# Kernel optimization log

Measured on AMD Instinct MI355X. Metric: run time of the kernel, lower is better.

## Reference

```python
import jax, jax.numpy as jnp
import numpy as np

B, T, C, H = 2, 2048, 1024, 16
D = C // H  # 64 per-head dim


def setup_inputs() -> dict:
    key = jax.random.key(0)
    ks = jax.random.split(key, 9)
    s = 1.0 / np.sqrt(C)
    return {
        "query_src": jax.random.normal(ks[0], (B, T, C), jnp.float32),
        "key_src": jax.random.normal(ks[1], (B, T, C), jnp.float32),
        "value_src": jax.random.normal(ks[2], (B, T, C), jnp.float32),
        "Wq": jax.random.normal(ks[3], (C, C), jnp.float32) * s,
        "Wk": jax.random.normal(ks[4], (C, C), jnp.float32) * s,
        "Wv": jax.random.normal(ks[5], (C, C), jnp.float32) * s,
        "Wo": jax.random.normal(ks[6], (C, C), jnp.float32) * s,
        "bo": jax.random.normal(ks[7], (C,), jnp.float32) * s,
    }


def reference(query_src, key_src, value_src, Wq, Wk, Wv, Wo, bo):
    # Linear layers: y = x @ W.T (torch nn.Linear convention)
    q = jnp.einsum('btc,dc->btd', query_src, Wq).reshape(B, T, H, D).transpose(0, 2, 1, 3)
    k = jnp.einsum('btc,dc->btd', key_src, Wk).reshape(B, T, H, D).transpose(0, 2, 1, 3)
    v = jnp.einsum('btc,dc->btd', value_src, Wv).reshape(B, T, H, D).transpose(0, 2, 1, 3)
    # scores: [B, H, T, T]
    scores = jnp.einsum('bhqd,bhkd->bhqk', q, k)
    # FAITHFUL quirk: original divides by d**(-0.5) => multiplies by sqrt(D)
    scores = scores * jnp.sqrt(jnp.asarray(D, scores.dtype))
    # FAITHFUL quirk: softmax over dim=1 == the HEAD axis
    attn = jax.nn.softmax(scores, axis=1)
    # dropout is identity in eval mode
    out = jnp.einsum('bhqk,bhkd->bhqd', attn, v)  # [B,H,T,D]
    out = out.transpose(0, 2, 1, 3).reshape(B, T, C)
    return jnp.einsum('btc,dc->btd', out, Wo) + bo
```

## Files before the change

### kernel.cpp

```cpp
#include <hip/hip_runtime.h>
#include <cmath>

namespace {

constexpr int B_ = 2;
constexpr int T_ = 2048;
constexpr int C_ = 1024;
constexpr int H_ = 16;
constexpr int D_ = 64;

typedef _Float16 half8 __attribute__((ext_vector_type(8)));
typedef _Float16 half4 __attribute__((ext_vector_type(4)));
typedef float f32x4 __attribute__((ext_vector_type(4)));

__device__ inline f32x4 vmax4(f32x4 a, f32x4 b) {
  f32x4 r;
  r[0] = fmaxf(a[0], b[0]); r[1] = fmaxf(a[1], b[1]);
  r[2] = fmaxf(a[2], b[2]); r[3] = fmaxf(a[3], b[3]);
  return r;
}

__device__ __forceinline__ void gload16(const _Float16* g, _Float16* l) {
  __builtin_amdgcn_global_load_lds(
      (const __attribute__((address_space(1))) unsigned int*)g,
      (__attribute__((address_space(3))) unsigned int*)l, 16, 0, 0);
}

__global__ __launch_bounds__(256)
void cast7(const float* __restrict__ xq, const float* __restrict__ xk,
           const float* __restrict__ xv, const float* __restrict__ wq,
           const float* __restrict__ wk, const float* __restrict__ wv,
           const float* __restrict__ wo,
           _Float16* __restrict__ dxq, _Float16* __restrict__ dxk,
           _Float16* __restrict__ dxv, _Float16* __restrict__ dwq,
           _Float16* __restrict__ dwk, _Float16* __restrict__ dwv,
           _Float16* __restrict__ dwo) {
  constexpr size_t NX = (size_t)4 << 20;
  constexpr size_t NW = (size_t)1 << 20;
  size_t g = ((size_t)blockIdx.x * 256 + threadIdx.x) * 8;
  const float* s; _Float16* d; size_t off;
  if      (g <     NX)          { s = xq; d = dxq; off = g; }
  else if (g < 2 * NX)          { s = xk; d = dxk; off = g - NX; }
  else if (g < 3 * NX)          { s = xv; d = dxv; off = g - 2 * NX; }
  else if (g < 3 * NX + NW)     { s = wq; d = dwq; off = g - 3 * NX; }
  else if (g < 3 * NX + 2 * NW) { s = wk; d = dwk; off = g - 3 * NX - NW; }
  else if (g < 3 * NX + 3 * NW) { s = wv; d = dwv; off = g - 3 * NX - 2 * NW; }
  else                          { s = wo; d = dwo; off = g - 3 * NX - 3 * NW; }
  const float4 a = *(const float4*)(s + off);
  const float4 b = *(const float4*)(s + off + 4);
  half8 h;
  h[0] = (_Float16)a.x; h[1] = (_Float16)a.y; h[2] = (_Float16)a.z; h[3] = (_Float16)a.w;
  h[4] = (_Float16)b.x; h[5] = (_Float16)b.y; h[6] = (_Float16)b.z; h[7] = (_Float16)b.w;
  *(half8*)(d + off) = h;
}

__global__ __launch_bounds__(256, 3)
void gemm_f16nt(const _Float16* __restrict__ A0, const _Float16* __restrict__ A1,
                const _Float16* __restrict__ A2,
                const _Float16* __restrict__ W0, const _Float16* __restrict__ W1,
                const _Float16* __restrict__ W2,
                _Float16* __restrict__ Y0, _Float16* __restrict__ Y1,
                _Float16* __restrict__ Y2,
                float* __restrict__ Yf, const float* __restrict__ bias,
                int K, int N, int mode) {
  __shared__ _Float16 sA[128 * 32];
  __shared__ _Float16 sW[128 * 32];

  const int tid  = threadIdx.x;
  const int lane = tid & 63;
  const int w    = tid >> 6;
  const int l15  = lane & 15;
  const int quad = lane >> 4;
  const int z    = blockIdx.z;
  const _Float16* A = (z == 0) ? A0 : (z == 1) ? A1 : A2;
  const _Float16* W = (z == 0) ? W0 : (z == 1) ? W1 : W2;
  _Float16*       Y = (z == 0) ? Y0 : (z == 1) ? Y1 : Y2;

  const int m0 = blockIdx.y * 128;
  const int n0 = blockIdx.x * 128;

  const int Rb  = lane >> 2;
  const int pch = lane & 3;
  const int lch = pch ^ ((Rb >> 1) & 3);
  const int swr = (l15 >> 1) & 3;

  f32x4 acc[4][4];
#pragma unroll
  for (int mt = 0; mt < 4; ++mt)
#pragma unroll
    for (int nt = 0; nt < 4; ++nt)
      acc[mt][nt] = (f32x4){0.f, 0.f, 0.f, 0.f};

  const int wm = (w >> 1) * 64;
  const int wn = (w & 1) * 64;

  for (int k0 = 0; k0 < K; k0 += 32) {
    __syncthreads();
#pragma unroll
    for (int j = 0; j < 2; ++j) {
      const int seg = w * 32 + j * 16;
      gload16(A + (size_t)(m0 + seg + Rb) * K + k0 + lch * 8, &sA[seg * 32]);
      gload16(W + (size_t)(n0 + seg + Rb) * K + k0 + lch * 8, &sW[seg * 32]);
    }
    __syncthreads();

    half8 af[4], wf[4];
#pragma unroll
    for (int mt = 0; mt < 4; ++mt) {
      const int R = wm + mt * 16 + l15;
      af[mt] = *(const half8*)&sA[R * 32 + (quad ^ swr) * 8];
    }
#pragma unroll
    for (int nt = 0; nt < 4; ++nt) {
      const int R = wn + nt * 16 + l15;
      wf[nt] = *(const half8*)&sW[R * 32 + (quad ^ swr) * 8];
    }
#pragma unroll
    for (int mt = 0; mt < 4; ++mt)
#pragma unroll
      for (int nt = 0; nt < 4; ++nt)
        acc[mt][nt] = __builtin_amdgcn_mfma_f32_16x16x32_f16(wf[nt], af[mt], acc[mt][nt], 0, 0, 0);
  }

#pragma unroll
  for (int mt = 0; mt < 4; ++mt)
#pragma unroll
    for (int nt = 0; nt < 4; ++nt) {
      const int m = m0 + wm + mt * 16 + l15;
      const int n = n0 + wn + nt * 16 + quad * 4;
      if (mode == 2) {
        float4 v;
        v.x = acc[mt][nt][0] + bias[n + 0];
        v.y = acc[mt][nt][1] + bias[n + 1];
        v.z = acc[mt][nt][2] + bias[n + 2];
        v.w = acc[mt][nt][3] + bias[n + 3];
        *(float4*)(Yf + (size_t)m * N + n) = v;
      } else {
        half4 hv;
#pragma unroll
        for (int r = 0; r < 4; ++r) hv[r] = (_Float16)acc[mt][nt][r];
        *(half4*)(Y + (size_t)m * N + n) = hv;
      }
    }
}

__global__ __launch_bounds__(256)
void transpose_v(const _Float16* __restrict__ Vh, _Float16* __restrict__ Vt) {
  constexpr int PAD = 1028;
  __shared__ _Float16 tile[16][PAD];
  const int b  = blockIdx.x >> 7;
  const int kt = blockIdx.x & 127;
  const int tid = threadIdx.x;

#pragma unroll
  for (int j = 0; j < 8; ++j) {
    const int ch = tid + 256 * j;
    const int t  = ch >> 7;
    const int c8 = ch & 127;
    *(half8*)&tile[t][c8 * 8] =
        *(const half8*)(Vh + ((size_t)b * T_ + kt * 16 + t) * C_ + c8 * 8);
  }
  __syncthreads();

#pragma unroll
  for (int j = 0; j < 8; ++j) {
    const int cc = tid + 256 * j;
    const int h  = cc >> 7;
    const int d  = (cc >> 1) & 63;
    const int th = (cc & 1) * 8;
    half8 v;
#pragma unroll
    for (int i = 0; i < 8; ++i) v[i] = tile[th + i][h * 64 + d];
    *(half8*)(Vt + ((((size_t)b * H_ + h) * 128 + kt) * 64 + d) * 16 + th) = v;
  }
}

__global__ __launch_bounds__(256, 2)
void attn_mfma(const _Float16* __restrict__ Qhp, const _Float16* __restrict__ Khp,
               const _Float16* __restrict__ Vtp, _Float16* __restrict__ OP,
               int nsplit) {
  __shared__ f32x4 red[2][2][4][64];

  const int tid  = threadIdx.x;
  const int lane = tid & 63;
  const int w    = tid >> 6;
  const int l15  = lane & 15;
  const int quad = lane >> 4;
  const int cell = quad * 16 + l15;

  const int nbq   = B_ * (T_ / 16);
  const int split = blockIdx.x / nbq;
  const int bq    = blockIdx.x % nbq;
  const int b  = bq >> 7;
  const int q0 = (bq & 127) << 4;

  const size_t qrow = ((size_t)b * T_ + q0 + l15) * C_;

  half8 qh[4][2];
#pragma unroll
  for (int hl = 0; hl < 4; ++hl)
#pragma unroll
    for (int kk = 0; kk < 2; ++kk)
      qh[hl][kk] = *(const half8*)(Qhp + qrow + (w * 4 + hl) * 64 + kk * 32 + quad * 8);

  f32x4 oacc[4][4];
#pragma unroll
  for (int hl = 0; hl < 4; ++hl)
#pragma unroll
    for (int mt = 0; mt < 4; ++mt)
      oacc[hl][mt] = (f32x4){0.f, 0.f, 0.f, 0.f};

  const int kpb  = T_ / nsplit;
  const int k_lo = split * kpb;
  const int jt   = kpb / 16;

  for (int j = 0; j < jt; ++j) {
    const int k0 = k_lo + j * 16;
    const int p  = j & 1;
    const int kt = k0 >> 4;
    const size_t krow = ((size_t)b * T_ + k0 + l15) * C_;

    half8 akh[4][2];
    half4 avf[4][4];
#pragma unroll
    for (int hl = 0; hl < 4; ++hl)
#pragma unroll
      for (int kk = 0; kk < 2; ++kk)
        akh[hl][kk] = *(const half8*)(Khp + krow + (w * 4 + hl) * 64 + kk * 32 + quad * 8);
#pragma unroll
    for (int hl = 0; hl < 4; ++hl) {
      const _Float16* vb =
          Vtp + (((size_t)b * H_ + (w * 4 + hl)) * 128 + kt) * 1024;
#pragma unroll
      for (int mt = 0; mt < 4; ++mt)
        avf[hl][mt] = *(const half4*)(vb + (mt * 16 + l15) * 16 + quad * 4);
    }

    f32x4 s[4];
#pragma unroll
    for (int hl = 0; hl < 4; ++hl) s[hl] = (f32x4){0.f, 0.f, 0.f, 0.f};
#pragma unroll
    for (int hl = 0; hl < 4; ++hl)
#pragma unroll
      for (int kk = 0; kk < 2; ++kk)
        s[hl] = __builtin_amdgcn_mfma_f32_16x16x32_f16(akh[hl][kk], qh[hl][kk], s[hl], 0, 0, 0);
#pragma unroll
    for (int hl = 0; hl < 4; ++hl) s[hl] = s[hl] * 8.f;

    red[p][0][w][cell] = vmax4(vmax4(s[0], s[1]), vmax4(s[2], s[3]));
    __syncthreads();
    const f32x4 gmax = vmax4(vmax4(red[p][0][0][cell], red[p][0][1][cell]),
                             vmax4(red[p][0][2][cell], red[p][0][3][cell]));
    float e[4][4];
    f32x4 ps = (f32x4){0.f, 0.f, 0.f, 0.f};
#pragma unroll
    for (int hl = 0; hl < 4; ++hl)
#pragma unroll
      for (int r = 0; r < 4; ++r) {
        e[hl][r] = __expf(s[hl][r] - gmax[r]);
        ps[r] += e[hl][r];
      }
    red[p][1][w][cell] = ps;
    __syncthreads();
    const f32x4 gs = red[p][1][0][cell] + red[p][1][1][cell] +
                     red[p][1][2][cell] + red[p][1][3][cell];
    f32x4 inv;
#pragma unroll
    for (int r = 0; r < 4; ++r) inv[r] = 1.f / gs[r];

    half4 pf[4];
#pragma unroll
    for (int hl = 0; hl < 4; ++hl)
#pragma unroll
      for (int r = 0; r < 4; ++r)
        pf[hl][r] = (_Float16)(e[hl][r] * inv[r]);

#pragma unroll
    for (int hl = 0; hl < 4; ++hl)
#pragma unroll
      for (int mt = 0; mt < 4; ++mt)
        oacc[hl][mt] =
            __builtin_amdgcn_mfma_f32_16x16x16f16(avf[hl][mt], pf[hl], oacc[hl][mt], 0, 0, 0);
  }

  _Float16* op = OP + (size_t)split * ((size_t)B_ * T_ * C_);
  const size_t orow = ((size_t)b * T_ + q0 + l15) * C_;
#pragma unroll
  for (int hl = 0; hl < 4; ++hl)
#pragma unroll
    for (int mt = 0; mt < 4; ++mt) {
      half4 hv;
#pragma unroll
      for (int r = 0; r < 4; ++r) hv[r] = (_Float16)oacc[hl][mt][r];
      *(half4*)(op + orow + (w * 4 + hl) * 64 + mt * 16 + quad * 4) = hv;
    }
}

__global__ __launch_bounds__(256)
void reduce_oh(const _Float16* __restrict__ OP, _Float16* __restrict__ AOh,
               int nsplit, size_t n) {
  const size_t i = ((size_t)blockIdx.x * 256 + threadIdx.x) * 8;
  float a[8] = {};
  for (int s = 0; s < nsplit; ++s) {
    const half8 v = *(const half8*)(OP + (size_t)s * n + i);
#pragma unroll
    for (int r = 0; r < 8; ++r) a[r] += (float)v[r];
  }
  half8 o;
#pragma unroll
  for (int r = 0; r < 8; ++r) o[r] = (_Float16)a[r];
  *(half8*)(AOh + i) = o;
}

}

extern "C" void kernel_launch(void* const* d_in, const int* in_sizes, int n_in,
                              void* d_out, int out_size, void* d_ws, size_t ws_size,
                              hipStream_t stream) {
  const float* xq = (const float*)d_in[0];
  const float* xk = (const float*)d_in[1];
  const float* xv = (const float*)d_in[2];
  const float* Wq = (const float*)d_in[3];
  const float* Wk = (const float*)d_in[4];
  const float* Wv = (const float*)d_in[5];
  const float* Wo = (const float*)d_in[6];
  const float* bo = (const float*)d_in[7];
  float* out = (float*)d_out;

  const size_t MB   = 1ull << 20;
  const size_t nBTC = (size_t)B_ * T_ * C_;

  char* wsb = (char*)d_ws;
  _Float16* Qh  = (_Float16*)(wsb + 0 * MB);
  _Float16* Kh  = (_Float16*)(wsb + 8 * MB);
  _Float16* Vt  = (_Float16*)(wsb + 16 * MB);
  _Float16* vh  = (_Float16*)(wsb + 24 * MB);
  _Float16* AOh = (_Float16*)(wsb + 24 * MB);
  _Float16* xqh = (_Float16*)(wsb + 32 * MB);
  _Float16* xkh = (_Float16*)(wsb + 40 * MB);
  _Float16* xvh = (_Float16*)(wsb + 48 * MB);
  _Float16* OP  = (_Float16*)(wsb + 32 * MB);
  _Float16* Wqh = (_Float16*)(wsb + 64 * MB);
  _Float16* Wkh = (_Float16*)(wsb + 66 * MB);
  _Float16* Wvh = (_Float16*)(wsb + 68 * MB);
  _Float16* Woh = (_Float16*)(wsb + 70 * MB);

  const int nsplit = 4;
  const int M = B_ * T_;
  dim3 blk(256);

  cast7<<<dim3(8192), blk, 0, stream>>>(xq, xk, xv, Wq, Wk, Wv, Wo,
                                        xqh, xkh, xvh, Wqh, Wkh, Wvh, Woh);

  gemm_f16nt<<<dim3(C_ / 128, M / 128, 3), blk, 0, stream>>>(
      xqh, xkh, xvh, Wqh, Wkh, Wvh, Qh, Kh, vh,
      nullptr, nullptr, C_, C_, 0);

  transpose_v<<<dim3(B_ * 128), blk, 0, stream>>>(vh, Vt);

  attn_mfma<<<dim3(B_ * (T_ / 16) * nsplit), blk, 0, stream>>>(Qh, Kh, Vt, OP, nsplit);

  reduce_oh<<<dim3((unsigned)(nBTC / 2048)), blk, 0, stream>>>(OP, AOh, nsplit, nBTC);

  gemm_f16nt<<<dim3(C_ / 128, M / 128, 1), blk, 0, stream>>>(
      AOh, nullptr, nullptr, Woh, nullptr, nullptr, nullptr, nullptr, nullptr,
      out, bo, C_, C_, 2);
}
```

Measured before the change: 390.8 us.

## Prefetch K tiles, repack V^T for 16-byte loads, and prioritize MFMA

Restructures the attention main loop to double-buffer K-tile register loads, issuing the next tile's loads before the softmax reductions so their latency overlaps the barriers. The V transpose kernel now writes a permuted layout so each lane fetches its four 16x16 V fragments with two 16-byte loads instead of sixteen 8-byte loads. It also adds s_setprio around the MFMA blocks and reuses the score registers for the exponentials. The extra buffer raises register pressure, and the unrolled-by-two loop assumes an even tile count per split.

```diff
diff --git a/kernel.cpp b/kernel.cpp
--- a/kernel.cpp
+++ b/kernel.cpp
@@ -168,10 +168,16 @@
     const int h  = cc >> 7;
     const int d  = (cc >> 1) & 63;
     const int th = (cc & 1) * 8;
-    half8 v;
-#pragma unroll
-    for (int i = 0; i < 8; ++i) v[i] = tile[th + i][h * 64 + d];
-    *(half8*)(Vt + ((((size_t)b * H_ + h) * 128 + kt) * 64 + d) * 16 + th) = v;
+    const int c  = h * 64 + d;
+    half4 va, vb4;
+#pragma unroll
+    for (int i = 0; i < 4; ++i) va[i]  = tile[th + i][c];
+#pragma unroll
+    for (int i = 0; i < 4; ++i) vb4[i] = tile[th + 4 + i][c];
+    const size_t base = (((size_t)b * H_ + h) * 128 + kt) * 1024 +
+                        (size_t)((d & 15) * 64 + (th >> 2) * 16 + (d >> 4) * 4);
+    *(half4*)(Vt + base) = va;
+    *(half4*)(Vt + base + 16) = vb4;
   }
 }
 
@@ -214,51 +220,61 @@
   const int k_lo = split * kpb;
   const int jt   = kpb / 16;
 
-  for (int j = 0; j < jt; ++j) {
+  const _Float16* vbase = Vtp + ((size_t)b * H_ + w * 4) * (128 * 1024) +
+                          (size_t)(l15 * 64 + quad * 16);
+
+  half8 akA[4][2], akB[4][2];
+
+  auto loadK = [&](half8 (&buf)[4][2], int k0) {
+    const size_t krow = ((size_t)b * T_ + k0 + l15) * C_;
+#pragma unroll
+    for (int hl = 0; hl < 4; ++hl)
+#pragma unroll
+      for (int kk = 0; kk < 2; ++kk)
+        buf[hl][kk] = *(const half8*)(Khp + krow + (w * 4 + hl) * 64 + kk * 32 + quad * 8);
+  };
+
+  auto tile = [&](int j, half8 (&cur)[4][2], half8 (&nxt)[4][2]) {
     const int k0 = k_lo + j * 16;
+    const int kt = k0 >> 4;
     const int p  = j & 1;
-    const int kt = k0 >> 4;
-    const size_t krow = ((size_t)b * T_ + k0 + l15) * C_;
-
-    half8 akh[4][2];
-    half4 avf[4][4];
+
+    f32x4 s[4];
+#pragma unroll
+    for (int hl = 0; hl < 4; ++hl) s[hl] = (f32x4){0.f, 0.f, 0.f, 0.f};
+    __builtin_amdgcn_s_setprio(1);
 #pragma unroll
     for (int hl = 0; hl < 4; ++hl)
 #pragma unroll
       for (int kk = 0; kk < 2; ++kk)
-        akh[hl][kk] = *(const half8*)(Khp + krow + (w * 4 + hl) * 64 + kk * 32 + quad * 8);
+        s[hl] = __builtin_amdgcn_mfma_f32_16x16x32_f16(cur[hl][kk], qh[hl][kk], s[hl], 0, 0, 0);
+    __builtin_amdgcn_s_setprio(0);
+#pragma unroll
+    for (int hl = 0; hl < 4; ++hl) s[hl] = s[hl] * 8.f;
+
+    half8 avh[4][2];
 #pragma unroll
     for (int hl = 0; hl < 4; ++hl) {
-      const _Float16* vb =
-          Vtp + (((size_t)b * H_ + (w * 4 + hl)) * 128 + kt) * 1024;
-#pragma unroll
-      for (int mt = 0; mt < 4; ++mt)
-        avf[hl][mt] = *(const half4*)(vb + (mt * 16 + l15) * 16 + quad * 4);
-    }
-
-    f32x4 s[4];
-#pragma unroll
-    for (int hl = 0; hl < 4; ++hl) s[hl] = (f32x4){0.f, 0.f, 0.f, 0.f};
-#pragma unroll
-    for (int hl = 0; hl < 4; ++hl)
-#pragma unroll
-      for (int kk = 0; kk < 2; ++kk)
-        s[hl] = __builtin_amdgcn_mfma_f32_16x16x32_f16(akh[hl][kk], qh[hl][kk], s[hl], 0, 0, 0);
-#pragma unroll
-    for (int hl = 0; hl < 4; ++hl) s[hl] = s[hl] * 8.f;
+      const _Float16* vb = vbase + (size_t)hl * (128 * 1024) + (size_t)kt * 1024;
+      avh[hl][0] = *(const half8*)(vb);
+      avh[hl][1] = *(const half8*)(vb + 8);
+    }
+    __builtin_amdgcn_sched_barrier(0);
+    if (j + 1 < jt) loadK(nxt, k0 + 16);
+    __builtin_amdgcn_sched_barrier(0);
 
     red[p][0][w][cell] = vmax4(vmax4(s[0], s[1]), vmax4(s[2], s[3]));
     __syncthreads();
     const f32x4 gmax = vmax4(vmax4(red[p][0][0][cell], red[p][0][1][cell]),
                              vmax4(red[p][0][2][cell], red[p][0][3][cell]));
-    float e[4][4];
     f32x4 ps = (f32x4){0.f, 0.f, 0.f, 0.f};
 #pragma unroll
     for (int hl = 0; hl < 4; ++hl)
 #pragma unroll
       for (int r = 0; r < 4; ++r) {
-        e[hl][r] = __expf(s[hl][r] - gmax[r]);
-        ps[r] += e[hl][r];
+        const float ev = __expf(s[hl][r] - gmax[r]);
+        s[hl][r] = ev;
+        ps[r] += ev;
       }
     red[p][1][w][cell] = ps;
     __syncthreads();
@@ -273,14 +289,27 @@
     for (int hl = 0; hl < 4; ++hl)
 #pragma unroll
       for (int r = 0; r < 4; ++r)
-        pf[hl][r] = (_Float16)(e[hl][r] * inv[r]);
-
-#pragma unroll
-    for (int hl = 0; hl < 4; ++hl)
-#pragma unroll
-      for (int mt = 0; mt < 4; ++mt)
-        oacc[hl][mt] =
-            __builtin_amdgcn_mfma_f32_16x16x16f16(avf[hl][mt], pf[hl], oacc[hl][mt], 0, 0, 0);
+        pf[hl][r] = (_Float16)(s[hl][r] * inv[r]);
+
+    __builtin_amdgcn_s_setprio(1);
+#pragma unroll
+    for (int hl = 0; hl < 4; ++hl) {
+      const half4 v0 = __builtin_shufflevector(avh[hl][0], avh[hl][0], 0, 1, 2, 3);
+      const half4 v1 = __builtin_shufflevector(avh[hl][0], avh[hl][0], 4, 5, 6, 7);
+      const half4 v2 = __builtin_shufflevector(avh[hl][1], avh[hl][1], 0, 1, 2, 3);
+      const half4 v3 = __builtin_shufflevector(avh[hl][1], avh[hl][1], 4, 5, 6, 7);
+      oacc[hl][0] = __builtin_amdgcn_mfma_f32_16x16x16f16(v0, pf[hl], oacc[hl][0], 0, 0, 0);
+      oacc[hl][1] = __builtin_amdgcn_mfma_f32_16x16x16f16(v1, pf[hl], oacc[hl][1], 0, 0, 0);
+      oacc[hl][2] = __builtin_amdgcn_mfma_f32_16x16x16f16(v2, pf[hl], oacc[hl][2], 0, 0, 0);
+      oacc[hl][3] = __builtin_amdgcn_mfma_f32_16x16x16f16(v3, pf[hl], oacc[hl][3], 0, 0, 0);
+    }
+    __builtin_amdgcn_s_setprio(0);
+  };
+
+  loadK(akA, k_lo);
+  for (int j = 0; j < jt; j += 2) {
+    tile(j,     akA, akB);
+    tile(j + 1, akB, akA);
   }
 
   _Float16* op = OP + (size_t)split * ((size_t)B_ * T_ * C_);
```

Result: slower. 424.0 us (+8.5%).
